# Kernel optimization log

Measured on AMD Instinct MI355X. Metric: run time of the kernel, lower is better.

The kernel has to match this reference:

```python
import jax, jax.numpy as jnp
import numpy as np

# w_mul = gain * 5**-0.5 * lrmul with gain=sqrt(2), use_wscale=True, lrmul=1
W_MUL = float(2 ** 0.5 * 5 ** -0.5)


def _apply_1q(M, g, q):
    """Apply 2x2 gate g on qubit q (MSB-first) to the rows of matrix M (dim, dim)."""
    dim = M.shape[0]
    Mr = M.reshape(2 ** q, 2, -1)  # (pre, 2, post*dim)
    return jnp.einsum('ab,xby->xay', g, Mr).reshape(dim, dim)


def _fused_xyz_gates(th, n):
    """Per-qubit fused gate Rz(tz) @ Ry(ty) @ Rx(tx); th = [tx_0..n, ty_0..n, tz_0..n]."""
    hx, hy, hz = th[:n] / 2, th[n:2 * n] / 2, th[2 * n:] / 2
    cx, sx = jnp.cos(hx), jnp.sin(hx)
    cy, sy = jnp.cos(hy), jnp.sin(hy)
    z = jnp.zeros_like(hz)
    gx = jnp.stack([jnp.stack([cx + 0j, -1j * sx], -1),
                    jnp.stack([-1j * sx, cx + 0j], -1)], -2)
    gy = jnp.stack([jnp.stack([cy + 0j, -sy + 0j], -1),
                    jnp.stack([sy + 0j, cy + 0j], -1)], -2)
    ez = jnp.exp(-1j * hz)
    gz = jnp.stack([jnp.stack([ez, z + 0j], -1),
                    jnp.stack([z + 0j, jnp.conj(ez)], -1)], -2)
    return jnp.einsum('nab,nbc,ncd->nad', gz, gy, gx).astype(jnp.complex64)


def _cnot_perm(n, c, t):
    """Row permutation implementing CNOT(control=c, target=t), MSB-first bit order."""
    r = np.arange(2 ** n)
    return r ^ (((r >> (n - 1 - c)) & 1) << (n - 1 - t))


def _build_U(weight):
    n = weight.shape[0] // 15
    dim = 2 ** n
    w = weight * W_MUL
    ring_perms = [jnp.asarray(_cnot_perm(n, c, (c + 1) % n)) for c in range(n)]
    U = jnp.eye(dim, dtype=jnp.complex64)
    for layer in range(5):  # 5 XYZ layers, rings of CNOT between them
        g = _fused_xyz_gates(w[3 * n * layer:3 * n * (layer + 1)], n)
        for q in range(n):
            U = _apply_1q(U, g[q], q)
        if layer < 4:
            for p in ring_perms:
                U = U[p]  # CNOT is a row permutation
    return U


def setup_inputs() -> dict:
    key = jax.random.key(0)
    k1, k2 = jax.random.split(key)
    n_qubits = 11
    dim = 2 ** n_qubits
    x = jax.random.normal(k1, (dim, dim), dtype=jnp.float32)
    weight = jax.random.uniform(k2, (15 * n_qubits,), dtype=jnp.float32,
                                minval=0.0, maxval=2.0 * np.pi)
    return {"x": x, "weight": weight}


def reference(x, weight):
    U = _build_U(weight)
    xc = x.astype(jnp.complex64)
    return U @ xc @ U.conj().T
```

## Files before the change

kernel.cpp:

```cpp
#include <hip/hip_runtime.h>

typedef unsigned short u16;
typedef __attribute__((ext_vector_type(8))) short bf16x8;
typedef __attribute__((ext_vector_type(4))) float f32x4;
typedef __attribute__((ext_vector_type(4))) unsigned int u32x4;

#define DIM 2048

__device__ inline u16 f2bf(float f) {
    unsigned u = __builtin_bit_cast(unsigned, f);
    u = (u + 0x7FFFu + ((u >> 16) & 1u)) >> 16;
    return (u16)u;
}

__device__ inline void gl_lds16(const void* g, void* l) {
    __builtin_amdgcn_global_load_lds(
        (const __attribute__((address_space(1))) unsigned int*)g,
        (__attribute__((address_space(3))) unsigned int*)l, 16, 0, 0);
}

struct c32 { float x, y; };
__device__ inline c32 cmul(c32 a, c32 b) { return {a.x*b.x - a.y*b.y, a.x*b.y + a.y*b.x}; }
__device__ inline float2 cmulf2(float2 a, float2 b) {
    return make_float2(a.x*b.x - a.y*b.y, a.x*b.y + a.y*b.x);
}

__device__ inline int slot2(int i) { return i + (i >> 4); }

__device__ inline void bfly(float2 g0, float2 g1, float2 g2, float2 g3,
                            float2& u, float2& w) {
    float2 nu, nw;
    nu.x = g0.x*u.x - g0.y*u.y + g1.x*w.x - g1.y*w.y;
    nu.y = g0.x*u.y + g0.y*u.x + g1.x*w.y + g1.y*w.x;
    nw.x = g2.x*u.x - g2.y*u.y + g3.x*w.x - g3.y*w.y;
    nw.y = g2.x*u.y + g2.y*u.x + g3.x*w.y + g3.y*w.x;
    u = nu; w = nw;
}

__global__ __launch_bounds__(256) void build_ut(const float* __restrict__ w,
                                                u16* __restrict__ ut_re,
                                                u16* __restrict__ ut_im) {
    __shared__ alignas(16) float2 gg[55][4];
    __shared__ alignas(16) u16 ptab[DIM];
    __shared__ alignas(16) float2 V[DIM + (DIM >> 4)];
    const int tid = threadIdx.x;
    const int col = blockIdx.x;

    if (tid < 55) {
        const int layer = tid / 11, q = tid - layer * 11;
        const float WM = 0.63245553203367586f;
        float hx = 0.5f * WM * w[33*layer + q];
        float hy = 0.5f * WM * w[33*layer + 11 + q];
        float hz = 0.5f * WM * w[33*layer + 22 + q];
        float cx = cosf(hx), sx = sinf(hx);
        float cy = cosf(hy), sy = sinf(hy);
        float cz = cosf(hz), sz = sinf(hz);
        c32 m00{cy*cx,  sy*sx}, m01{-sy*cx, -cy*sx};
        c32 m10{sy*cx, -cy*sx}, m11{ cy*cx, -sy*sx};
        c32 em{cz, -sz}, ep{cz, sz};
        c32 r0 = cmul(em, m00), r1 = cmul(em, m01);
        c32 r2 = cmul(ep, m10), r3 = cmul(ep, m11);
        gg[tid][0] = make_float2(r0.x, r0.y);
        gg[tid][1] = make_float2(r1.x, r1.y);
        gg[tid][2] = make_float2(r2.x, r2.y);
        gg[tid][3] = make_float2(r3.x, r3.y);
    }
    for (int i = tid; i < DIM; i += 256) {
        int jj = (i ^ (i >> 1)) ^ ((i & 1) ? 0x600 : 0);
        ptab[i] = (u16)slot2(jj);
    }
    __syncthreads();

    {
        float2 p = gg[0][((((tid >> 7) & 1) << 1)) | ((col >> 10) & 1)];
        #pragma unroll
        for (int b = 9; b >= 3; --b) {
            float2 ge = gg[10 - b][(((tid >> (b - 3)) & 1) << 1) | ((col >> b) & 1)];
            p = cmulf2(p, ge);
        }
        const int c2 = (col >> 2) & 1, c1 = (col >> 1) & 1, c0 = col & 1;
        float2 a0  = cmulf2(p, gg[8][c2]);
        float2 a1  = cmulf2(p, gg[8][2 | c2]);
        float2 b00 = cmulf2(a0, gg[9][c1]);
        float2 b01 = cmulf2(a0, gg[9][2 | c1]);
        float2 b10 = cmulf2(a1, gg[9][c1]);
        float2 b11 = cmulf2(a1, gg[9][2 | c1]);
        float2 g0 = gg[10][c0], g1 = gg[10][2 | c0];
        const int base = tid << 3;
        V[slot2(base + 0)] = cmulf2(b00, g0);
        V[slot2(base + 1)] = cmulf2(b00, g1);
        V[slot2(base + 2)] = cmulf2(b01, g0);
        V[slot2(base + 3)] = cmulf2(b01, g1);
        V[slot2(base + 4)] = cmulf2(b10, g0);
        V[slot2(base + 5)] = cmulf2(b10, g1);
        V[slot2(base + 6)] = cmulf2(b11, g0);
        V[slot2(base + 7)] = cmulf2(b11, g1);
    }
    __syncthreads();

    auto round3 = [&](int b2, int b1, int b0, int gq2, int gq1, int gq0,
                      bool permRead) {
        int x = tid;
        x = ((x >> b0) << (b0 + 1)) | (x & ((1 << b0) - 1));
        x = ((x >> b1) << (b1 + 1)) | (x & ((1 << b1) - 1));
        x = ((x >> b2) << (b2 + 1)) | (x & ((1 << b2) - 1));
        float2 v[8]; int sl[8];
        #pragma unroll
        for (int j = 0; j < 8; ++j) {
            int e = x | ((j >> 2) << b2) | (((j >> 1) & 1) << b1) | ((j & 1) << b0);
            sl[j] = slot2(e);
            v[j] = V[permRead ? (int)ptab[e] : sl[j]];
        }
        if (permRead) __syncthreads();
        {   float2 g0 = gg[gq2][0], g1 = gg[gq2][1], g2 = gg[gq2][2], g3 = gg[gq2][3];
            bfly(g0,g1,g2,g3, v[0], v[4]); bfly(g0,g1,g2,g3, v[1], v[5]);
            bfly(g0,g1,g2,g3, v[2], v[6]); bfly(g0,g1,g2,g3, v[3], v[7]); }
        {   float2 g0 = gg[gq1][0], g1 = gg[gq1][1], g2 = gg[gq1][2], g3 = gg[gq1][3];
            bfly(g0,g1,g2,g3, v[0], v[2]); bfly(g0,g1,g2,g3, v[1], v[3]);
            bfly(g0,g1,g2,g3, v[4], v[6]); bfly(g0,g1,g2,g3, v[5], v[7]); }
        {   float2 g0 = gg[gq0][0], g1 = gg[gq0][1], g2 = gg[gq0][2], g3 = gg[gq0][3];
            bfly(g0,g1,g2,g3, v[0], v[1]); bfly(g0,g1,g2,g3, v[2], v[3]);
            bfly(g0,g1,g2,g3, v[4], v[5]); bfly(g0,g1,g2,g3, v[6], v[7]); }
        #pragma unroll
        for (int j = 0; j < 8; ++j) V[sl[j]] = v[j];
        __syncthreads();
    };

    auto round2 = [&](int gq1, int gq0) {
        float2 g10 = gg[gq1][0], g11 = gg[gq1][1], g12 = gg[gq1][2], g13 = gg[gq1][3];
        float2 g00 = gg[gq0][0], g01 = gg[gq0][1], g02 = gg[gq0][2], g03 = gg[gq0][3];
        #pragma unroll
        for (int h = 0; h < 2; ++h) {
            int i0 = (tid + h * 256) << 2;
            float2 v[4]; int sl[4];
            #pragma unroll
            for (int j = 0; j < 4; ++j) { sl[j] = slot2(i0 | j); v[j] = V[sl[j]]; }
            bfly(g10,g11,g12,g13, v[0], v[2]); bfly(g10,g11,g12,g13, v[1], v[3]);
            bfly(g00,g01,g02,g03, v[0], v[1]); bfly(g00,g01,g02,g03, v[2], v[3]);
            #pragma unroll
            for (int j = 0; j < 4; ++j) V[sl[j]] = v[j];
        }
        __syncthreads();
    };

    for (int layer = 1; layer < 5; ++layer) {
        const int gb = layer * 11;
        round3(10, 9, 8, gb + 0, gb + 1, gb + 2, true);
        round3( 7, 6, 5, gb + 3, gb + 4, gb + 5, false);
        round3( 4, 3, 2, gb + 6, gb + 7, gb + 8, false);
        round2(gb + 9, gb + 10);
    }
    for (int i = tid; i < DIM; i += 256) {
        float2 v = V[slot2(i)];
        ut_re[(size_t)col*DIM + i] = f2bf(v.x);
        ut_im[(size_t)col*DIM + i] = f2bf(v.y);
    }
}

__global__ __launch_bounds__(256) void transpose2(const u16* __restrict__ sre,
                                                  const u16* __restrict__ sim,
                                                  u16* __restrict__ dre,
                                                  u16* __restrict__ dim_) {
    const u16* s = blockIdx.z ? sim : sre;
    u16*       d = blockIdx.z ? dim_ : dre;
    __shared__ alignas(16) u16 tile[64][66];
    const int bx = blockIdx.x * 64, by = blockIdx.y * 64;
    for (int e = threadIdx.x; e < 1024; e += 256) {
        int r = e >> 4, c4 = (e & 15) * 4;
        uint2 v = *(const uint2*)(s + (size_t)(by + r) * DIM + bx + c4);
        u16* tp = &tile[r][c4];
        tp[0] = (u16)(v.x); tp[1] = (u16)(v.x >> 16);
        tp[2] = (u16)(v.y); tp[3] = (u16)(v.y >> 16);
    }
    __syncthreads();
    for (int e = threadIdx.x; e < 1024; e += 256) {
        int r = e >> 4, c4 = (e & 15) * 4;
        unsigned lo = (unsigned)tile[c4][r]     | ((unsigned)tile[c4+1][r] << 16);
        unsigned hi = (unsigned)tile[c4+2][r]   | ((unsigned)tile[c4+3][r] << 16);
        *(uint2*)(d + (size_t)(bx + r) * DIM + by + c4) = make_uint2(lo, hi);
    }
}

__global__ __launch_bounds__(256) void x2bf(const float* __restrict__ x,
                                            u16* __restrict__ xb) {
    const int i = (blockIdx.x * 256 + threadIdx.x) * 8;
    const float4* s = (const float4*)(x + i);
    float4 v0 = s[0], v1 = s[1];
    u32x4 pk;
    pk.x = (unsigned)f2bf(v0.x) | ((unsigned)f2bf(v0.y) << 16);
    pk.y = (unsigned)f2bf(v0.z) | ((unsigned)f2bf(v0.w) << 16);
    pk.z = (unsigned)f2bf(v1.x) | ((unsigned)f2bf(v1.y) << 16);
    pk.w = (unsigned)f2bf(v1.z) | ((unsigned)f2bf(v1.w) << 16);
    *(u32x4*)(xb + i) = pk;
}

__global__ __launch_bounds__(256, 2) void gemm_stage1(
        const u16* __restrict__ ure, const u16* __restrict__ uim,
        const u16* __restrict__ xb,
        u16* __restrict__ pt, u16* __restrict__ qt) {
    __shared__ alignas(16) u16 Ab[2][2][128*32], Bx[2][2][128*32];
    const u16* A  = blockIdx.z ? uim : ure;
    u16*      dst = blockIdx.z ? qt  : pt;
    const int tid  = threadIdx.x;
    const int lane = tid & 63, w = tid >> 6;
    const int m0 = blockIdx.y * 128, n0 = blockIdx.x * 128;
    const int wm = (w >> 1) * 64, wn = (w & 1) * 64;
    const int ml = lane & 15, quad = lane >> 4;

    f32x4 acc[4][4];
    #pragma unroll
    for (int i = 0; i < 4; ++i)
        #pragma unroll
        for (int j = 0; j < 4; ++j) {
            f32x4 z = {0.f, 0.f, 0.f, 0.f};
            acc[i][j] = z;
        }

    auto stage = [&](int b, int k0) {
        #pragma unroll
        for (int pn = 0; pn < 2; ++pn) {
            #pragma unroll
            for (int t = 0; t < 2; ++t) {
                int ci = t * 256 + tid;
                int r = ci >> 2, c = ci & 3;
                size_t goA = ((size_t)(m0 + r) * DIM + k0 + pn * 32) * 2 + c * 16;
                size_t goB = ((size_t)(n0 + r) * DIM + k0 + pn * 32) * 2 + c * 16;
                gl_lds16((const char*)A  + goA, (char*)Ab[b][pn] + ci * 16);
                gl_lds16((const char*)xb + goB, (char*)Bx[b][pn] + ci * 16);
            }
        }
    };

    stage(0, 0);
    __syncthreads();

    for (int k0 = 0; k0 < DIM; k0 += 64) {
        const int cb = (k0 >> 6) & 1;
        if (k0 + 64 < DIM) stage(cb ^ 1, k0 + 64);

        #pragma unroll
        for (int pn = 0; pn < 2; ++pn) {
            bf16x8 af[4], bf[4];
            #pragma unroll
            for (int i = 0; i < 4; ++i) {
                af[i] = *(const bf16x8*)(Ab[cb][pn] + (wm + i*16 + ml) * 32 + quad * 8);
                bf[i] = *(const bf16x8*)(Bx[cb][pn] + (wn + i*16 + ml) * 32 + quad * 8);
            }
            #pragma unroll
            for (int i = 0; i < 4; ++i)
                #pragma unroll
                for (int j = 0; j < 4; ++j)
                    acc[i][j] = __builtin_amdgcn_mfma_f32_16x16x32_bf16(af[i], bf[j], acc[i][j], 0, 0, 0);
        }
        __syncthreads();
    }
    #pragma unroll
    for (int i = 0; i < 4; ++i)
        #pragma unroll
        for (int j = 0; j < 4; ++j) {
            int row = m0 + wm + i*16 + quad*4;
            int col = n0 + wn + j*16 + ml;
            #pragma unroll
            for (int r = 0; r < 4; ++r)
                dst[(size_t)(row + r) * DIM + col] = f2bf(acc[i][j][r]);
        }
}

__global__ __launch_bounds__(256, 2) void gemm_stage2_atomic(
        const u16* __restrict__ ure, const u16* __restrict__ uim,
        const u16* __restrict__ pt, const u16* __restrict__ qt,
        float* __restrict__ out) {
    __shared__ alignas(16) u16 Ab[2][2][128*32], Bb[2][2][128*32];
    const u16* A = blockIdx.z ? uim : ure;
    const u16* B = blockIdx.z ? qt  : pt;
    const int tid  = threadIdx.x;
    const int lane = tid & 63, w = tid >> 6;
    const int m0 = blockIdx.y * 128, n0 = blockIdx.x * 128;
    const int wm = (w >> 1) * 64, wn = (w & 1) * 64;
    const int ml = lane & 15, quad = lane >> 4;

    f32x4 acc[4][4];
    #pragma unroll
    for (int i = 0; i < 4; ++i)
        #pragma unroll
        for (int j = 0; j < 4; ++j) {
            f32x4 z = {0.f, 0.f, 0.f, 0.f};
            acc[i][j] = z;
        }

    auto stage = [&](int b, int k0) {
        #pragma unroll
        for (int pn = 0; pn < 2; ++pn) {
            #pragma unroll
            for (int t = 0; t < 2; ++t) {
                int ci = t * 256 + tid;
                int r = ci >> 2, c = ci & 3;
                size_t goA = ((size_t)(m0 + r) * DIM + k0 + pn * 32) * 2 + c * 16;
                size_t goB = ((size_t)(n0 + r) * DIM + k0 + pn * 32) * 2 + c * 16;
                gl_lds16((const char*)A + goA, (char*)Ab[b][pn] + ci * 16);
                gl_lds16((const char*)B + goB, (char*)Bb[b][pn] + ci * 16);
            }
        }
    };

    stage(0, 0);
    __syncthreads();

    for (int k0 = 0; k0 < DIM; k0 += 64) {
        const int cb = (k0 >> 6) & 1;
        if (k0 + 64 < DIM) stage(cb ^ 1, k0 + 64);

        #pragma unroll
        for (int pn = 0; pn < 2; ++pn) {
            bf16x8 af[4], bf[4];
            #pragma unroll
            for (int i = 0; i < 4; ++i) {
                af[i] = *(const bf16x8*)(Ab[cb][pn] + (wm + i*16 + ml) * 32 + quad * 8);
                bf[i] = *(const bf16x8*)(Bb[cb][pn] + (wn + i*16 + ml) * 32 + quad * 8);
            }
            #pragma unroll
            for (int i = 0; i < 4; ++i)
                #pragma unroll
                for (int j = 0; j < 4; ++j)
                    acc[i][j] = __builtin_amdgcn_mfma_f32_16x16x32_bf16(af[i], bf[j], acc[i][j], 0, 0, 0);
        }
        __syncthreads();
    }
    #pragma unroll
    for (int i = 0; i < 4; ++i)
        #pragma unroll
        for (int j = 0; j < 4; ++j) {
            int row = m0 + wm + i*16 + quad*4;
            int col = n0 + wn + j*16 + ml;
            #pragma unroll
            for (int r = 0; r < 4; ++r)
                unsafeAtomicAdd(&out[(size_t)(row + r) * DIM + col], acc[i][j][r]);
        }
}

__global__ __launch_bounds__(256, 1) void gemm_stage2_cplx(
        const u16* __restrict__ ure, const u16* __restrict__ uim,
        const u16* __restrict__ pt, const u16* __restrict__ qt,
        float2* __restrict__ out, size_t out_lim) {
    __shared__ alignas(16) u16 Ar[128*32], Ai[128*32], Bp[128*32], Bq[128*32];
    const int tid  = threadIdx.x;
    const int lane = tid & 63, w = tid >> 6;
    const int m0 = blockIdx.y * 128, n0 = blockIdx.x * 128;
    const int wm = (w >> 1) * 64, wn = (w & 1) * 64;
    const int ml = lane & 15, quad = lane >> 4;

    f32x4 accR[4][4], accI[4][4];
    #pragma unroll
    for (int i = 0; i < 4; ++i)
        #pragma unroll
        for (int j = 0; j < 4; ++j) {
            f32x4 z = {0.f, 0.f, 0.f, 0.f};
            accR[i][j] = z; accI[i][j] = z;
        }

    for (int k0 = 0; k0 < DIM; k0 += 32) {
        #pragma unroll
        for (int t = 0; t < 2; ++t) {
            int ci = t * 256 + tid;
            int r = ci >> 2, c = ci & 3;
            size_t goA = ((size_t)(m0 + r) * DIM + k0) * 2 + c * 16;
            size_t goB = ((size_t)(n0 + r) * DIM + k0) * 2 + c * 16;
            gl_lds16((const char*)ure + goA, (char*)Ar + ci * 16);
            gl_lds16((const char*)uim + goA, (char*)Ai + ci * 16);
            gl_lds16((const char*)pt  + goB, (char*)Bp + ci * 16);
            gl_lds16((const char*)qt  + goB, (char*)Bq + ci * 16);
        }
        __syncthreads();
        bf16x8 ar[4], ai[4], bp[4], bq[4];
        #pragma unroll
        for (int i = 0; i < 4; ++i) {
            ar[i] = *(const bf16x8*)(Ar + (wm + i*16 + ml) * 32 + quad * 8);
            ai[i] = *(const bf16x8*)(Ai + (wm + i*16 + ml) * 32 + quad * 8);
            bp[i] = *(const bf16x8*)(Bp + (wn + i*16 + ml) * 32 + quad * 8);
            bq[i] = *(const bf16x8*)(Bq + (wn + i*16 + ml) * 32 + quad * 8);
        }
        #pragma unroll
        for (int i = 0; i < 4; ++i)
            #pragma unroll
            for (int j = 0; j < 4; ++j) {
                accR[i][j] = __builtin_amdgcn_mfma_f32_16x16x32_bf16(ar[i], bp[j], accR[i][j], 0, 0, 0);
                accR[i][j] = __builtin_amdgcn_mfma_f32_16x16x32_bf16(ai[i], bq[j], accR[i][j], 0, 0, 0);
                accI[i][j] = __builtin_amdgcn_mfma_f32_16x16x32_bf16(ai[i], bp[j], accI[i][j], 0, 0, 0);
                f32x4 t2 = __builtin_amdgcn_mfma_f32_16x16x32_bf16(ar[i], bq[j], {0.f,0.f,0.f,0.f}, 0, 0, 0);
                accI[i][j] -= t2;
            }
        __syncthreads();
    }
    #pragma unroll
    for (int i = 0; i < 4; ++i)
        #pragma unroll
        for (int j = 0; j < 4; ++j) {
            int row = m0 + wm + i*16 + quad*4;
            int col = n0 + wn + j*16 + ml;
            #pragma unroll
            for (int r = 0; r < 4; ++r) {
                size_t idx = (size_t)(row + r) * DIM + col;
                if (idx < out_lim)
                    out[idx] = make_float2(accR[i][j][r], accI[i][j][r]);
            }
        }
}

extern "C" void kernel_launch(void* const* d_in, const int* in_sizes, int n_in,
                              void* d_out, int out_size, void* d_ws, size_t ws_size,
                              hipStream_t stream) {
    int xi = (in_sizes[0] >= in_sizes[1]) ? 0 : 1;
    const float* x = (const float*)d_in[xi];
    const float* w = (const float*)d_in[1 - xi];

    char* ws = (char*)d_ws;
    const size_t P = (size_t)DIM * DIM * 2;
    if (ws_size < 4 * P) return;

    u16* ut_re = (u16*)(ws);
    u16* ut_im = (u16*)(ws + P);
    u16* u_re  = (u16*)(ws + 2*P);
    u16* u_im  = (u16*)(ws + 3*P);
    u16* pt    = ut_re;
    u16* qt    = ut_im;
    u16* xb = (ws_size >= 5 * P) ? (u16*)(ws + 4*P) : (u16*)d_out;

    build_ut<<<DIM, 256, 0, stream>>>(w, ut_re, ut_im);
    transpose2<<<dim3(32, 32, 2), 256, 0, stream>>>(ut_re, ut_im, u_re, u_im);
    x2bf<<<DIM*DIM/(256*8), 256, 0, stream>>>(x, xb);
    gemm_stage1<<<dim3(16, 16, 2), 256, 0, stream>>>(u_re, u_im, xb, pt, qt);

    if (out_size == DIM * DIM) {
        hipMemsetAsync(d_out, 0, (size_t)DIM * DIM * sizeof(float), stream);
        gemm_stage2_atomic<<<dim3(16, 16, 2), 256, 0, stream>>>(u_re, u_im, pt, qt,
                                                                (float*)d_out);
    } else {
        gemm_stage2_cplx<<<dim3(16, 16), 256, 0, stream>>>(u_re, u_im, pt, qt,
                                                           (float2*)d_out,
                                                           (size_t)out_size / 2);
    }
}
```

Baseline: 246.0 us.

## Use wave shuffles in U build and fuse stage-2 real/imag GEMMs without atomics

The unitary-build kernel now applies five of the per-qubit butterflies with cross-lane shuffles inside a wave instead of LDS round trips. This removes the permutation table and several barrier-separated rounds, and the bf16 output is written directly from registers as vector stores. Stage 2 now runs the real and imaginary K halves in one block over a 2*DIM K loop and does plain stores, which drops the memset and the float atomics. The trade-off is half as many blocks in stage 2, so there is less parallelism across the GPU.

```diff
diff --git a/kernel.cpp b/kernel.cpp
--- a/kernel.cpp
+++ b/kernel.cpp
@@ -26,6 +26,10 @@
 }
 
 __device__ inline int slot2(int i) { return i + (i >> 4); }
+
+__device__ inline float2 shflx2(float2 v, int m) {
+    return make_float2(__shfl_xor(v.x, m, 64), __shfl_xor(v.y, m, 64));
+}
 
 __device__ inline void bfly(float2 g0, float2 g1, float2 g2, float2 g3,
                             float2& u, float2& w) {
@@ -41,10 +45,10 @@
                                                 u16* __restrict__ ut_re,
                                                 u16* __restrict__ ut_im) {
     __shared__ alignas(16) float2 gg[55][4];
-    __shared__ alignas(16) u16 ptab[DIM];
     __shared__ alignas(16) float2 V[DIM + (DIM >> 4)];
-    const int tid = threadIdx.x;
-    const int col = blockIdx.x;
+    const int tid  = threadIdx.x;
+    const int lane = tid & 63;
+    const int col  = blockIdx.x;
 
     if (tid < 55) {
         const int layer = tid / 11, q = tid - layer * 11;
@@ -65,10 +69,6 @@
         gg[tid][2] = make_float2(r2.x, r2.y);
         gg[tid][3] = make_float2(r3.x, r3.y);
     }
-    for (int i = tid; i < DIM; i += 256) {
-        int jj = (i ^ (i >> 1)) ^ ((i & 1) ? 0x600 : 0);
-        ptab[i] = (u16)slot2(jj);
-    }
     __syncthreads();
 
     {
@@ -86,74 +86,96 @@
         float2 b10 = cmulf2(a1, gg[9][c1]);
         float2 b11 = cmulf2(a1, gg[9][2 | c1]);
         float2 g0 = gg[10][c0], g1 = gg[10][2 | c0];
-        const int base = tid << 3;
-        V[slot2(base + 0)] = cmulf2(b00, g0);
-        V[slot2(base + 1)] = cmulf2(b00, g1);
-        V[slot2(base + 2)] = cmulf2(b01, g0);
-        V[slot2(base + 3)] = cmulf2(b01, g1);
-        V[slot2(base + 4)] = cmulf2(b10, g0);
-        V[slot2(base + 5)] = cmulf2(b10, g1);
-        V[slot2(base + 6)] = cmulf2(b11, g0);
-        V[slot2(base + 7)] = cmulf2(b11, g1);
+        const int sb = slot2(tid << 3);
+        V[sb + 0] = cmulf2(b00, g0);
+        V[sb + 1] = cmulf2(b00, g1);
+        V[sb + 2] = cmulf2(b01, g0);
+        V[sb + 3] = cmulf2(b01, g1);
+        V[sb + 4] = cmulf2(b10, g0);
+        V[sb + 5] = cmulf2(b10, g1);
+        V[sb + 6] = cmulf2(b11, g0);
+        V[sb + 7] = cmulf2(b11, g1);
     }
     __syncthreads();
-
-    auto round3 = [&](int b2, int b1, int b0, int gq2, int gq1, int gq0,
-                      bool permRead) {
-        int x = tid;
-        x = ((x >> b0) << (b0 + 1)) | (x & ((1 << b0) - 1));
-        x = ((x >> b1) << (b1 + 1)) | (x & ((1 << b1) - 1));
-        x = ((x >> b2) << (b2 + 1)) | (x & ((1 << b2) - 1));
-        float2 v[8]; int sl[8];
-        #pragma unroll
-        for (int j = 0; j < 8; ++j) {
-            int e = x | ((j >> 2) << b2) | (((j >> 1) & 1) << b1) | ((j & 1) << b0);
-            sl[j] = slot2(e);
-            v[j] = V[permRead ? (int)ptab[e] : sl[j]];
-        }
-        if (permRead) __syncthreads();
-        {   float2 g0 = gg[gq2][0], g1 = gg[gq2][1], g2 = gg[gq2][2], g3 = gg[gq2][3];
-            bfly(g0,g1,g2,g3, v[0], v[4]); bfly(g0,g1,g2,g3, v[1], v[5]);
-            bfly(g0,g1,g2,g3, v[2], v[6]); bfly(g0,g1,g2,g3, v[3], v[7]); }
-        {   float2 g0 = gg[gq1][0], g1 = gg[gq1][1], g2 = gg[gq1][2], g3 = gg[gq1][3];
-            bfly(g0,g1,g2,g3, v[0], v[2]); bfly(g0,g1,g2,g3, v[1], v[3]);
-            bfly(g0,g1,g2,g3, v[4], v[6]); bfly(g0,g1,g2,g3, v[5], v[7]); }
-        {   float2 g0 = gg[gq0][0], g1 = gg[gq0][1], g2 = gg[gq0][2], g3 = gg[gq0][3];
-            bfly(g0,g1,g2,g3, v[0], v[1]); bfly(g0,g1,g2,g3, v[2], v[3]);
-            bfly(g0,g1,g2,g3, v[4], v[5]); bfly(g0,g1,g2,g3, v[6], v[7]); }
-        #pragma unroll
-        for (int j = 0; j < 8; ++j) V[sl[j]] = v[j];
-        __syncthreads();
-    };
-
-    auto round2 = [&](int gq1, int gq0) {
-        float2 g10 = gg[gq1][0], g11 = gg[gq1][1], g12 = gg[gq1][2], g13 = gg[gq1][3];
-        float2 g00 = gg[gq0][0], g01 = gg[gq0][1], g02 = gg[gq0][2], g03 = gg[gq0][3];
-        #pragma unroll
-        for (int h = 0; h < 2; ++h) {
-            int i0 = (tid + h * 256) << 2;
-            float2 v[4]; int sl[4];
-            #pragma unroll
-            for (int j = 0; j < 4; ++j) { sl[j] = slot2(i0 | j); v[j] = V[sl[j]]; }
-            bfly(g10,g11,g12,g13, v[0], v[2]); bfly(g10,g11,g12,g13, v[1], v[3]);
-            bfly(g00,g01,g02,g03, v[0], v[1]); bfly(g00,g01,g02,g03, v[2], v[3]);
-            #pragma unroll
-            for (int j = 0; j < 4; ++j) V[sl[j]] = v[j];
-        }
-        __syncthreads();
-    };
 
     for (int layer = 1; layer < 5; ++layer) {
         const int gb = layer * 11;
-        round3(10, 9, 8, gb + 0, gb + 1, gb + 2, true);
-        round3( 7, 6, 5, gb + 3, gb + 4, gb + 5, false);
-        round3( 4, 3, 2, gb + 6, gb + 7, gb + 8, false);
-        round2(gb + 9, gb + 10);
-    }
-    for (int i = tid; i < DIM; i += 256) {
-        float2 v = V[slot2(i)];
-        ut_re[(size_t)col*DIM + i] = f2bf(v.x);
-        ut_im[(size_t)col*DIM + i] = f2bf(v.y);
+
+        {
+            float2 a[8]; int sl[8];
+            #pragma unroll
+            for (int j = 0; j < 8; ++j) {
+                int e  = tid | (j << 8);
+                sl[j]  = slot2(e);
+                int pe = (e ^ (e >> 1)) ^ ((e & 1) ? 0x600 : 0);
+                a[j]   = V[slot2(pe)];
+            }
+            __syncthreads();
+            {   float2 g0 = gg[gb+0][0], g1 = gg[gb+0][1], g2 = gg[gb+0][2], g3 = gg[gb+0][3];
+                bfly(g0,g1,g2,g3, a[0], a[4]); bfly(g0,g1,g2,g3, a[1], a[5]);
+                bfly(g0,g1,g2,g3, a[2], a[6]); bfly(g0,g1,g2,g3, a[3], a[7]); }
+            {   float2 g0 = gg[gb+1][0], g1 = gg[gb+1][1], g2 = gg[gb+1][2], g3 = gg[gb+1][3];
+                bfly(g0,g1,g2,g3, a[0], a[2]); bfly(g0,g1,g2,g3, a[1], a[3]);
+                bfly(g0,g1,g2,g3, a[4], a[6]); bfly(g0,g1,g2,g3, a[5], a[7]); }
+            {   float2 g0 = gg[gb+2][0], g1 = gg[gb+2][1], g2 = gg[gb+2][2], g3 = gg[gb+2][3];
+                bfly(g0,g1,g2,g3, a[0], a[1]); bfly(g0,g1,g2,g3, a[2], a[3]);
+                bfly(g0,g1,g2,g3, a[4], a[5]); bfly(g0,g1,g2,g3, a[6], a[7]); }
+            #pragma unroll
+            for (int j = 0; j < 8; ++j) V[sl[j]] = a[j];
+            __syncthreads();
+        }
+
+        {
+            const int sb = slot2(tid << 3);
+            float2 v[8];
+            #pragma unroll
+            for (int j = 0; j < 8; ++j) v[j] = V[sb + j];
+
+            #pragma unroll
+            for (int b = 7; b >= 3; --b) {
+                const int gq = gb + (10 - b);
+                const int m  = 1 << (b - 3);
+                const bool hi = (lane & m) != 0;
+                float2 g0 = gg[gq][0], g1 = gg[gq][1], g2 = gg[gq][2], g3 = gg[gq][3];
+                float2 ca = hi ? g3 : g0;
+                float2 cb = hi ? g2 : g1;
+                #pragma unroll
+                for (int j = 0; j < 8; ++j) {
+                    float2 p = shflx2(v[j], m);
+                    float2 o = v[j];
+                    v[j].x = ca.x*o.x - ca.y*o.y + cb.x*p.x - cb.y*p.y;
+                    v[j].y = ca.x*o.y + ca.y*o.x + cb.x*p.y + cb.y*p.x;
+                }
+            }
+            {   float2 g0 = gg[gb+8][0], g1 = gg[gb+8][1], g2 = gg[gb+8][2], g3 = gg[gb+8][3];
+                bfly(g0,g1,g2,g3, v[0], v[4]); bfly(g0,g1,g2,g3, v[1], v[5]);
+                bfly(g0,g1,g2,g3, v[2], v[6]); bfly(g0,g1,g2,g3, v[3], v[7]); }
+            {   float2 g0 = gg[gb+9][0], g1 = gg[gb+9][1], g2 = gg[gb+9][2], g3 = gg[gb+9][3];
+                bfly(g0,g1,g2,g3, v[0], v[2]); bfly(g0,g1,g2,g3, v[1], v[3]);
+                bfly(g0,g1,g2,g3, v[4], v[6]); bfly(g0,g1,g2,g3, v[5], v[7]); }
+            {   float2 g0 = gg[gb+10][0], g1 = gg[gb+10][1], g2 = gg[gb+10][2], g3 = gg[gb+10][3];
+                bfly(g0,g1,g2,g3, v[0], v[1]); bfly(g0,g1,g2,g3, v[2], v[3]);
+                bfly(g0,g1,g2,g3, v[4], v[5]); bfly(g0,g1,g2,g3, v[6], v[7]); }
+
+            if (layer < 4) {
+                #pragma unroll
+                for (int j = 0; j < 8; ++j) V[sb + j] = v[j];
+                __syncthreads();
+            } else {
+                const int base = tid << 3;
+                u32x4 pr, pi;
+                pr.x = (unsigned)f2bf(v[0].x) | ((unsigned)f2bf(v[1].x) << 16);
+                pr.y = (unsigned)f2bf(v[2].x) | ((unsigned)f2bf(v[3].x) << 16);
+                pr.z = (unsigned)f2bf(v[4].x) | ((unsigned)f2bf(v[5].x) << 16);
+                pr.w = (unsigned)f2bf(v[6].x) | ((unsigned)f2bf(v[7].x) << 16);
+                pi.x = (unsigned)f2bf(v[0].y) | ((unsigned)f2bf(v[1].y) << 16);
+                pi.y = (unsigned)f2bf(v[2].y) | ((unsigned)f2bf(v[3].y) << 16);
+                pi.z = (unsigned)f2bf(v[4].y) | ((unsigned)f2bf(v[5].y) << 16);
+                pi.w = (unsigned)f2bf(v[6].y) | ((unsigned)f2bf(v[7].y) << 16);
+                *(u32x4*)(ut_re + (size_t)col * DIM + base) = pr;
+                *(u32x4*)(ut_im + (size_t)col * DIM + base) = pi;
+            }
+        }
     }
 }
 
@@ -266,13 +288,11 @@
         }
 }
 
-__global__ __launch_bounds__(256, 2) void gemm_stage2_atomic(
+__global__ __launch_bounds__(256, 2) void gemm_stage2_fused(
         const u16* __restrict__ ure, const u16* __restrict__ uim,
         const u16* __restrict__ pt, const u16* __restrict__ qt,
         float* __restrict__ out) {
     __shared__ alignas(16) u16 Ab[2][2][128*32], Bb[2][2][128*32];
-    const u16* A = blockIdx.z ? uim : ure;
-    const u16* B = blockIdx.z ? qt  : pt;
     const int tid  = threadIdx.x;
     const int lane = tid & 63, w = tid >> 6;
     const int m0 = blockIdx.y * 128, n0 = blockIdx.x * 128;
@@ -288,7 +308,10 @@
             acc[i][j] = z;
         }
 
-    auto stage = [&](int b, int k0) {
+    auto stage = [&](int b, int kk) {
+        const u16* A = (kk & DIM) ? uim : ure;
+        const u16* B = (kk & DIM) ? qt  : pt;
+        const int k0 = kk & (DIM - 1);
         #pragma unroll
         for (int pn = 0; pn < 2; ++pn) {
             #pragma unroll
@@ -306,9 +329,9 @@
     stage(0, 0);
     __syncthreads();
 
-    for (int k0 = 0; k0 < DIM; k0 += 64) {
-        const int cb = (k0 >> 6) & 1;
-        if (k0 + 64 < DIM) stage(cb ^ 1, k0 + 64);
+    for (int kk = 0; kk < 2 * DIM; kk += 64) {
+        const int cb = (kk >> 6) & 1;
+        if (kk + 64 < 2 * DIM) stage(cb ^ 1, kk + 64);
 
         #pragma unroll
         for (int pn = 0; pn < 2; ++pn) {
@@ -334,7 +357,7 @@
             int col = n0 + wn + j*16 + ml;
             #pragma unroll
             for (int r = 0; r < 4; ++r)
-                unsafeAtomicAdd(&out[(size_t)(row + r) * DIM + col], acc[i][j][r]);
+                out[(size_t)(row + r) * DIM + col] = acc[i][j][r];
         }
 }
 
@@ -431,9 +454,8 @@
     gemm_stage1<<<dim3(16, 16, 2), 256, 0, stream>>>(u_re, u_im, xb, pt, qt);
 
     if (out_size == DIM * DIM) {
-        hipMemsetAsync(d_out, 0, (size_t)DIM * DIM * sizeof(float), stream);
-        gemm_stage2_atomic<<<dim3(16, 16, 2), 256, 0, stream>>>(u_re, u_im, pt, qt,
-                                                                (float*)d_out);
+        gemm_stage2_fused<<<dim3(16, 16), 256, 0, stream>>>(u_re, u_im, pt, qt,
+                                                            (float*)d_out);
     } else {
         gemm_stage2_cplx<<<dim3(16, 16), 256, 0, stream>>>(u_re, u_im, pt, qt,
                                                            (float2*)d_out,
```

After: 249.5 us. Within noise of the previous version (+1.4%).
